# Performance work log

Hardware: AMD Instinct MI355X
Metric: run time of the kernel (lower is better)

The kernel has to match this reference:

```python
import jax, jax.numpy as jnp
import numpy as np
from functools import partial

D = 1024
H = 4 * D
E = 8
K_TOP = 2
B, T = 4, 2048
NEG_INF = jnp.float32(-1e30)


def setup_inputs() -> dict:
    key = jax.random.key(0)
    ks = jax.random.split(key, 12)
    s = 0.02
    return {
        "x": jax.random.normal(ks[0], (B, T, D), jnp.float32),
        "noise": jax.random.normal(ks[1], (B, T, E), jnp.float32),
        "gate_w": jax.random.normal(ks[2], (E, D), jnp.float32) * s,
        "gate_b": jnp.zeros((E,), jnp.float32),
        "var_w": jax.random.normal(ks[3], (E, D), jnp.float32) * s,
        "var_b": jnp.zeros((E,), jnp.float32),
        "w1": jax.random.normal(ks[4], (E, H, D), jnp.float32) * s,
        "b1": jnp.zeros((E, H), jnp.float32),
        "w2": jax.random.normal(ks[5], (E, D, H), jnp.float32) * s,
        "b2": jnp.zeros((E, D), jnp.float32),
    }


def reference(x, noise, gate_w, gate_b, var_w, var_b, w1, b1, w2, b2):
    # Noisy top-k gating
    logits = jnp.einsum("btd,ed->bte", x, gate_w) + gate_b          # [B,T,E]
    std = jax.nn.softplus(jnp.einsum("btd,ed->bte", x, var_w) + var_b)
    noisy = logits + noise * std                                      # [B,T,E]
    _, idx = jax.lax.top_k(noisy, K_TOP)                              # [B,T,K]
    # boolean top-k mask over experts
    mask = (idx[..., None] == jnp.arange(E)).any(axis=-2)             # [B,T,E]
    coef = jax.nn.softmax(jnp.where(mask, noisy, NEG_INF), axis=-1)   # zeros outside top-k

    # Combine: sum_e coef_e * FFN_e(x). coef is exactly 0 for non-selected
    # experts, so this equals the masked gather/scatter math. Scan over the
    # small expert dim to avoid a [E,B,T,H] intermediate.
    coef_e = jnp.moveaxis(coef, -1, 0)                                # [E,B,T]

    def body(acc, ew):
        w1e, b1e, w2e, b2e, ce = ew
        h = jax.nn.relu(jnp.einsum("btd,hd->bth", x, w1e) + b1e)
        y = jnp.einsum("bth,dh->btd", h, w2e) + b2e
        return acc + y * ce[..., None], None

    out, _ = jax.lax.scan(body, jnp.zeros_like(x), (w1, b1, w2, b2, coef_e))
    return out
```

## Files before the change

### kernel.cpp

```cpp
#include <hip/hip_runtime.h>
#include <hip/hip_bf16.h>
#include <math.h>

#define NTOK 8192
#define DD   1024
#define HH   4096
#define NE   8
#define SLOT_CAP 17408
#define BM 128
#define BN 128
#define BK 64

typedef __bf16 bf16;
typedef __bf16 bf16x8 __attribute__((ext_vector_type(8)));
typedef __bf16 bf16x4 __attribute__((ext_vector_type(4)));
typedef float  f32x4  __attribute__((ext_vector_type(4)));

typedef __attribute__((address_space(3))) unsigned char lds_u8;
typedef const __attribute__((address_space(1))) unsigned char g_u8;

__device__ __forceinline__ void gload16(const bf16* g, bf16* l) {
  __builtin_amdgcn_global_load_lds((g_u8*)g, (lds_u8*)l, 16, 0, 0);
}

__device__ __forceinline__ float softplus_f(float v) {
  return fmaxf(v, 0.f) + log1pf(expf(-fabsf(v)));
}

__global__ __launch_bounds__(64) void moe_gate_kernel(
    const float* __restrict__ x, const float* __restrict__ noise,
    const float* __restrict__ gate_w, const float* __restrict__ gate_b,
    const float* __restrict__ var_w,  const float* __restrict__ var_b,
    float* __restrict__ coef2, int* __restrict__ t2e, int* __restrict__ counts)
{
  const int t = blockIdx.x;
  const int lane = threadIdx.x;
  const float* xt = x + (size_t)t * DD;
  float pg[NE], pv[NE];
  #pragma unroll
  for (int e = 0; e < NE; ++e) { pg[e] = 0.f; pv[e] = 0.f; }
  #pragma unroll 4
  for (int i = 0; i < DD / 64; ++i) {
    const int d = lane + i * 64;
    const float xv = xt[d];
    #pragma unroll
    for (int e = 0; e < NE; ++e) {
      pg[e] = fmaf(xv, gate_w[e * DD + d], pg[e]);
      pv[e] = fmaf(xv, var_w[e * DD + d], pv[e]);
    }
  }
  #pragma unroll
  for (int e = 0; e < NE; ++e) {
    #pragma unroll
    for (int off = 32; off; off >>= 1) {
      pg[e] += __shfl_xor(pg[e], off);
      pv[e] += __shfl_xor(pv[e], off);
    }
  }
  if (lane == 0) {
    float noisy[NE];
    #pragma unroll
    for (int e = 0; e < NE; ++e) {
      const float lg = pg[e] + gate_b[e];
      const float sd = softplus_f(pv[e] + var_b[e]);
      noisy[e] = lg + noise[t * NE + e] * sd;
    }
    int i1 = 0; float n1 = noisy[0];
    #pragma unroll
    for (int e = 1; e < NE; ++e) if (noisy[e] > n1) { n1 = noisy[e]; i1 = e; }
    int i2 = -1; float n2 = -3.0e38f;
    #pragma unroll
    for (int e = 0; e < NE; ++e) if (e != i1 && noisy[e] > n2) { n2 = noisy[e]; i2 = e; }
    const float e2 = expf(n2 - n1);
    const float den = 1.f + e2;
    coef2[t * 2 + 0] = 1.f / den;
    coef2[t * 2 + 1] = e2 / den;
    t2e[t * 2 + 0] = i1;
    t2e[t * 2 + 1] = i2;
    atomicAdd(&counts[i1], 1);
    atomicAdd(&counts[i2], 1);
  }
}

__global__ void moe_offsets_kernel(const int* __restrict__ counts, int* __restrict__ po) {
  if (threadIdx.x == 0) {
    int acc = 0;
    po[0] = 0;
    for (int e = 0; e < NE; ++e) {
      acc += ((counts[e] + BM - 1) / BM) * BM;
      po[e + 1] = acc;
    }
  }
}

__global__ __launch_bounds__(256) void moe_scatter_kernel(
    const int* __restrict__ t2e, const float* __restrict__ coef2,
    const int* __restrict__ po, int* __restrict__ cnt2,
    int* __restrict__ assign_tok, float* __restrict__ slot_coef)
{
  const int t = blockIdx.x * 256 + threadIdx.x;
  if (t >= NTOK) return;
  #pragma unroll
  for (int k = 0; k < 2; ++k) {
    const int e = t2e[t * 2 + k];
    const int pos = atomicAdd(&cnt2[e], 1);
    const int slot = po[e] + pos;
    assign_tok[slot] = t;
    slot_coef[slot] = coef2[t * 2 + k];
  }
}

__global__ __launch_bounds__(256) void cvt_bf16_kernel(const float* __restrict__ src,
                                                       bf16* __restrict__ dst, int n4) {
  for (int i = blockIdx.x * 256 + threadIdx.x; i < n4; i += gridDim.x * 256) {
    const float4 f = ((const float4*)src)[i];
    bf16x4 v;
    v[0] = (bf16)f.x; v[1] = (bf16)f.y; v[2] = (bf16)f.z; v[3] = (bf16)f.w;
    ((bf16x4*)dst)[i] = v;
  }
}

__global__ __launch_bounds__(256) void moe_ffn1_kernel(
    const bf16* __restrict__ xb, const bf16* __restrict__ w1b, const float* __restrict__ b1,
    const int* __restrict__ assign_tok, const int* __restrict__ po,
    bf16* __restrict__ h, int chunk_base)
{
  __shared__ bf16 As[BM][BK];
  __shared__ bf16 Bs[BN][BK];
  __shared__ int toks[BM];
  const int po8 = po[NE];
  const int row0 = chunk_base + blockIdx.x * BM;
  if (row0 >= po8) return;
  int e = 0;
  while (row0 >= po[e + 1]) ++e;
  const int bn0 = blockIdx.y * BN;
  const bf16* w1e = w1b + (size_t)e * HH * DD;
  const int tid = threadIdx.x, lane = tid & 63, wave = tid >> 6;
  if (tid < BM) {
    const int s = assign_tok[row0 + tid];
    toks[tid] = s < 0 ? 0 : s;
  }
  __syncthreads();

  const int rin = lane >> 3;
  const int c8s = ((lane & 7) ^ rin) * 8;
  const bf16* asrc[4];
  const bf16* bsrc[4];
  #pragma unroll
  for (int i = 0; i < 4; ++i) {
    const int c = wave * 4 + i;
    const int row = c * 8 + rin;
    asrc[i] = xb + (size_t)toks[row] * DD + c8s;
    bsrc[i] = w1e + (size_t)(bn0 + row) * DD + c8s;
  }

  const int la = lane & 15, hi = lane >> 4;
  const int wm = (wave >> 1) * 64, wn = (wave & 1) * 64;
  f32x4 acc[4][4];
  #pragma unroll
  for (int m = 0; m < 4; ++m)
    #pragma unroll
    for (int n = 0; n < 4; ++n) acc[m][n] = {0.f, 0.f, 0.f, 0.f};

  for (int k0 = 0; k0 < DD; k0 += BK) {
    #pragma unroll
    for (int i = 0; i < 4; ++i) gload16(asrc[i] + k0, &As[(wave * 4 + i) * 8][0]);
    #pragma unroll
    for (int i = 0; i < 4; ++i) gload16(bsrc[i] + k0, &Bs[(wave * 4 + i) * 8][0]);
    __syncthreads();
    #pragma unroll
    for (int ks = 0; ks < 2; ++ks) {
      bf16x8 af[4], bff[4];
      #pragma unroll
      for (int m = 0; m < 4; ++m) {
        const int row = wm + m * 16 + la;
        const int c8 = (ks * 4 + hi) ^ (row & 7);
        af[m] = *(const bf16x8*)(&As[row][c8 * 8]);
      }
      #pragma unroll
      for (int n = 0; n < 4; ++n) {
        const int row = wn + n * 16 + la;
        const int c8 = (ks * 4 + hi) ^ (row & 7);
        bff[n] = *(const bf16x8*)(&Bs[row][c8 * 8]);
      }
      #pragma unroll
      for (int m = 0; m < 4; ++m)
        #pragma unroll
        for (int n = 0; n < 4; ++n)
          acc[m][n] = __builtin_amdgcn_mfma_f32_16x16x32_bf16(af[m], bff[n], acc[m][n], 0, 0, 0);
    }
    __syncthreads();
  }

  const int hrow0 = row0 - chunk_base;
  #pragma unroll
  for (int n = 0; n < 4; ++n) {
    const int col = bn0 + wn + n * 16 + la;
    const float bb = b1[e * HH + col];
    #pragma unroll
    for (int m = 0; m < 4; ++m) {
      const int rbase = wm + m * 16 + hi * 4;
      #pragma unroll
      for (int r = 0; r < 4; ++r) {
        float v = acc[m][n][r] + bb;
        v = v > 0.f ? v : 0.f;
        h[(size_t)(hrow0 + rbase + r) * HH + col] = (bf16)v;
      }
    }
  }
}

__global__ __launch_bounds__(256) void moe_ffn2_kernel(
    const bf16* __restrict__ h, const bf16* __restrict__ w2b, const float* __restrict__ b2,
    const int* __restrict__ assign_tok, const float* __restrict__ slot_coef,
    const int* __restrict__ po, float* __restrict__ out, int chunk_base)
{
  __shared__ bf16 As[BM][BK];
  __shared__ bf16 Bs[BN][BK];
  __shared__ int toks[BM];
  const int po8 = po[NE];
  const int row0 = chunk_base + blockIdx.x * BM;
  if (row0 >= po8) return;
  int e = 0;
  while (row0 >= po[e + 1]) ++e;
  const int bn0 = blockIdx.y * BN;
  const bf16* w2e = w2b + (size_t)e * DD * HH;
  const int tid = threadIdx.x, lane = tid & 63, wave = tid >> 6;
  if (tid < BM) toks[tid] = assign_tok[row0 + tid];
  __syncthreads();

  const int rin = lane >> 3;
  const int c8s = ((lane & 7) ^ rin) * 8;
  const bf16* asrc[4];
  const bf16* bsrc[4];
  const int arow0 = row0 - chunk_base;
  #pragma unroll
  for (int i = 0; i < 4; ++i) {
    const int c = wave * 4 + i;
    const int row = c * 8 + rin;
    asrc[i] = h + (size_t)(arow0 + row) * HH + c8s;
    bsrc[i] = w2e + (size_t)(bn0 + row) * HH + c8s;
  }

  const int la = lane & 15, hi = lane >> 4;
  const int wm = (wave >> 1) * 64, wn = (wave & 1) * 64;
  f32x4 acc[4][4];
  #pragma unroll
  for (int m = 0; m < 4; ++m)
    #pragma unroll
    for (int n = 0; n < 4; ++n) acc[m][n] = {0.f, 0.f, 0.f, 0.f};

  for (int k0 = 0; k0 < HH; k0 += BK) {
    #pragma unroll
    for (int i = 0; i < 4; ++i) gload16(asrc[i] + k0, &As[(wave * 4 + i) * 8][0]);
    #pragma unroll
    for (int i = 0; i < 4; ++i) gload16(bsrc[i] + k0, &Bs[(wave * 4 + i) * 8][0]);
    __syncthreads();
    #pragma unroll
    for (int ks = 0; ks < 2; ++ks) {
      bf16x8 af[4], bff[4];
      #pragma unroll
      for (int m = 0; m < 4; ++m) {
        const int row = wm + m * 16 + la;
        const int c8 = (ks * 4 + hi) ^ (row & 7);
        af[m] = *(const bf16x8*)(&As[row][c8 * 8]);
      }
      #pragma unroll
      for (int n = 0; n < 4; ++n) {
        const int row = wn + n * 16 + la;
        const int c8 = (ks * 4 + hi) ^ (row & 7);
        bff[n] = *(const bf16x8*)(&Bs[row][c8 * 8]);
      }
      #pragma unroll
      for (int m = 0; m < 4; ++m)
        #pragma unroll
        for (int n = 0; n < 4; ++n)
          acc[m][n] = __builtin_amdgcn_mfma_f32_16x16x32_bf16(af[m], bff[n], acc[m][n], 0, 0, 0);
    }
    __syncthreads();
  }

  #pragma unroll
  for (int n = 0; n < 4; ++n) {
    const int col = bn0 + wn + n * 16 + la;
    const float bb = b2[e * DD + col];
    #pragma unroll
    for (int m = 0; m < 4; ++m) {
      const int rbase = wm + m * 16 + hi * 4;
      #pragma unroll
      for (int r = 0; r < 4; ++r) {
        const int trow = rbase + r;
        const int tok = toks[trow];
        if (tok >= 0) {
          const float c = slot_coef[row0 + trow];
          atomicAdd(out + (size_t)tok * DD + col, c * (acc[m][n][r] + bb));
        }
      }
    }
  }
}

extern "C" void kernel_launch(void* const* d_in, const int* in_sizes, int n_in,
                              void* d_out, int out_size, void* d_ws, size_t ws_size,
                              hipStream_t stream) {
  const float* x      = (const float*)d_in[0];
  const float* noise  = (const float*)d_in[1];
  const float* gate_w = (const float*)d_in[2];
  const float* gate_b = (const float*)d_in[3];
  const float* var_w  = (const float*)d_in[4];
  const float* var_b  = (const float*)d_in[5];
  const float* w1     = (const float*)d_in[6];
  const float* b1     = (const float*)d_in[7];
  const float* w2     = (const float*)d_in[8];
  const float* b2     = (const float*)d_in[9];
  float* out = (float*)d_out;
  (void)in_sizes; (void)n_in; (void)out_size;

  char* ws = (char*)d_ws;
  size_t off = 0;
  auto alloc = [&](size_t bytes) {
    off = (off + 255) & ~(size_t)255;
    size_t o = off;
    off += bytes;
    return o;
  };
  bf16*  xb         = (bf16*)(ws + alloc((size_t)NTOK * DD * 2));
  float* coef2      = (float*)(ws + alloc((size_t)NTOK * 2 * 4));
  int*   t2e        = (int*)(ws + alloc((size_t)NTOK * 2 * 4));
  int*   counts     = (int*)(ws + alloc(64));
  int*   cnt2       = counts + 8;
  int*   po         = (int*)(ws + alloc(64));
  int*   assign_tok = (int*)(ws + alloc((size_t)SLOT_CAP * 4));
  float* slot_coef  = (float*)(ws + alloc((size_t)SLOT_CAP * 4));
  bf16*  w1b        = (bf16*)(ws + alloc((size_t)NE * HH * DD * 2));
  bf16*  w2b        = (bf16*)(ws + alloc((size_t)NE * DD * HH * 2));
  off = (off + 255) & ~(size_t)255;
  const size_t h_avail = ws_size > off ? ws_size - off : 0;
  int chunk_rows = (int)(h_avail / ((size_t)HH * 2));
  chunk_rows = (chunk_rows / BM) * BM;
  if (chunk_rows < BM) chunk_rows = BM;
  if (chunk_rows > SLOT_CAP) chunk_rows = SLOT_CAP;
  bf16* hbuf = (bf16*)(ws + off);

  hipMemsetAsync(counts, 0, 64, stream);
  hipMemsetAsync(assign_tok, 0xFF, (size_t)SLOT_CAP * 4, stream);
  hipMemsetAsync(out, 0, (size_t)NTOK * DD * 4, stream);

  moe_gate_kernel<<<NTOK, 64, 0, stream>>>(x, noise, gate_w, gate_b, var_w, var_b,
                                           coef2, t2e, counts);
  moe_offsets_kernel<<<1, 64, 0, stream>>>(counts, po);
  moe_scatter_kernel<<<NTOK / 256, 256, 0, stream>>>(t2e, coef2, po, cnt2,
                                                     assign_tok, slot_coef);
  cvt_bf16_kernel<<<2048, 256, 0, stream>>>(x, xb, NTOK * DD / 4);
  cvt_bf16_kernel<<<2048, 256, 0, stream>>>(w1, w1b, NE * HH * DD / 4);
  cvt_bf16_kernel<<<2048, 256, 0, stream>>>(w2, w2b, NE * DD * HH / 4);

  const int rounds = (SLOT_CAP + chunk_rows - 1) / chunk_rows;
  for (int r = 0; r < rounds; ++r) {
    const int cb = r * chunk_rows;
    const int rows_here = (cb + chunk_rows <= SLOT_CAP) ? chunk_rows : (SLOT_CAP - cb);
    dim3 g1(rows_here / BM, HH / BN);
    moe_ffn1_kernel<<<g1, 256, 0, stream>>>(xb, w1b, b1, assign_tok, po, hbuf, cb);
    dim3 g2(rows_here / BM, DD / BN);
    moe_ffn2_kernel<<<g2, 256, 0, stream>>>(hbuf, w2b, b2, assign_tok, slot_coef,
                                            po, out, cb);
  }
}
```

Measured before the change: 954.4 us.

## Use 256x256 double-buffered tiles with XCD-aware block remap in expert GEMMs

```diff
diff --git a/kernel.cpp b/kernel.cpp
--- a/kernel.cpp
+++ b/kernel.cpp
@@ -6,10 +6,10 @@
 #define DD   1024
 #define HH   4096
 #define NE   8
-#define SLOT_CAP 17408
-#define BM 128
-#define BN 128
+#define BM 256
+#define BN 256
 #define BK 64
+#define SLOT_CAP (2 * NTOK + NE * BM)
 
 typedef __bf16 bf16;
 typedef __bf16 bf16x8 __attribute__((ext_vector_type(8)));
@@ -120,180 +120,139 @@
   }
 }
 
-__global__ __launch_bounds__(256) void moe_ffn1_kernel(
-    const bf16* __restrict__ xb, const bf16* __restrict__ w1b, const float* __restrict__ b1,
-    const int* __restrict__ assign_tok, const int* __restrict__ po,
-    bf16* __restrict__ h, int chunk_base)
+template<int KDIM, int NCOLS, bool FFN1>
+__global__ __launch_bounds__(512, 2) void moe_gemm_kernel(
+    const bf16* __restrict__ Asrc, const bf16* __restrict__ Wsrc,
+    const float* __restrict__ bias,
+    const int* __restrict__ assign_tok, const float* __restrict__ slot_coef,
+    const int* __restrict__ po,
+    bf16* __restrict__ hout, float* __restrict__ out,
+    int chunk_base, int gx)
 {
-  __shared__ bf16 As[BM][BK];
-  __shared__ bf16 Bs[BN][BK];
+  __shared__ bf16 smA[2][BM * BK];
+  __shared__ bf16 smB[2][BN * BK];
   __shared__ int toks[BM];
+
+  const int nwg = gx * (NCOLS / BN);
+  const int lin = blockIdx.x;
+  const int q = nwg >> 3, r = nwg & 7;
+  const int xcd = lin & 7, idx = lin >> 3;
+  const int wg = (xcd < r ? xcd * (q + 1) : r * (q + 1) + (xcd - r) * q) + idx;
+  const int bx = wg % gx, by = wg / gx;
+
+  const int row0 = chunk_base + bx * BM;
   const int po8 = po[NE];
-  const int row0 = chunk_base + blockIdx.x * BM;
   if (row0 >= po8) return;
   int e = 0;
   while (row0 >= po[e + 1]) ++e;
-  const int bn0 = blockIdx.y * BN;
-  const bf16* w1e = w1b + (size_t)e * HH * DD;
-  const int tid = threadIdx.x, lane = tid & 63, wave = tid >> 6;
-  if (tid < BM) {
-    const int s = assign_tok[row0 + tid];
-    toks[tid] = s < 0 ? 0 : s;
-  }
+  const int bn0 = by * BN;
+  const bf16* We = Wsrc + (size_t)e * ((size_t)HH * DD);
+
+  const int tid = threadIdx.x, lane = tid & 63;
+  if (tid < BM) toks[tid] = assign_tok[row0 + tid];
   __syncthreads();
 
-  const int rin = lane >> 3;
-  const int c8s = ((lane & 7) ^ rin) * 8;
-  const bf16* asrc[4];
-  const bf16* bsrc[4];
+  const int t7 = tid & 7;
+  const bf16* aptr[4];
+  const bf16* bptr[4];
   #pragma unroll
   for (int i = 0; i < 4; ++i) {
-    const int c = wave * 4 + i;
-    const int row = c * 8 + rin;
-    asrc[i] = xb + (size_t)toks[row] * DD + c8s;
-    bsrc[i] = w1e + (size_t)(bn0 + row) * DD + c8s;
-  }
-
+    const int g = i * 512 + tid;
+    const int row = g >> 3;
+    const int c8 = ((t7 ^ (row & 7)) * 8);
+    int ar;
+    if constexpr (FFN1) {
+      const int s = toks[row];
+      ar = s < 0 ? 0 : s;
+    } else {
+      ar = row0 - chunk_base + row;
+    }
+    aptr[i] = Asrc + (size_t)ar * KDIM + c8;
+    bptr[i] = We + (size_t)(bn0 + row) * KDIM + c8;
+  }
+
+  auto stage = [&](int sel, int k0) {
+    #pragma unroll
+    for (int i = 0; i < 4; ++i)
+      gload16(aptr[i] + k0, &smA[sel][(i * 512 + tid) * 8]);
+    #pragma unroll
+    for (int i = 0; i < 4; ++i)
+      gload16(bptr[i] + k0, &smB[sel][(i * 512 + tid) * 8]);
+  };
+
+  const int wid = tid >> 6, wr = wid >> 2, wc = wid & 3;
   const int la = lane & 15, hi = lane >> 4;
-  const int wm = (wave >> 1) * 64, wn = (wave & 1) * 64;
-  f32x4 acc[4][4];
-  #pragma unroll
-  for (int m = 0; m < 4; ++m)
+  f32x4 acc[8][4];
+  #pragma unroll
+  for (int m = 0; m < 8; ++m)
     #pragma unroll
     for (int n = 0; n < 4; ++n) acc[m][n] = {0.f, 0.f, 0.f, 0.f};
 
-  for (int k0 = 0; k0 < DD; k0 += BK) {
-    #pragma unroll
-    for (int i = 0; i < 4; ++i) gload16(asrc[i] + k0, &As[(wave * 4 + i) * 8][0]);
-    #pragma unroll
-    for (int i = 0; i < 4; ++i) gload16(bsrc[i] + k0, &Bs[(wave * 4 + i) * 8][0]);
-    __syncthreads();
-    #pragma unroll
-    for (int ks = 0; ks < 2; ++ks) {
-      bf16x8 af[4], bff[4];
-      #pragma unroll
-      for (int m = 0; m < 4; ++m) {
-        const int row = wm + m * 16 + la;
-        const int c8 = (ks * 4 + hi) ^ (row & 7);
-        af[m] = *(const bf16x8*)(&As[row][c8 * 8]);
+  constexpr int NK = KDIM / BK;
+  stage(0, 0);
+  __syncthreads();
+  #pragma unroll 2
+  for (int ks = 0; ks < NK; ++ks) {
+    const int cur = ks & 1;
+    if (ks + 1 < NK) stage(cur ^ 1, (ks + 1) * BK);
+    const bf16* A = smA[cur];
+    const bf16* B = smB[cur];
+    #pragma unroll
+    for (int kk = 0; kk < 2; ++kk) {
+      bf16x8 af[8], bf_[4];
+      #pragma unroll
+      for (int m = 0; m < 8; ++m) {
+        const int rw = wr * 128 + m * 16 + la;
+        const int c8 = ((kk * 4 + hi) ^ (rw & 7)) * 8;
+        af[m] = *(const bf16x8*)(A + rw * 64 + c8);
       }
       #pragma unroll
       for (int n = 0; n < 4; ++n) {
-        const int row = wn + n * 16 + la;
-        const int c8 = (ks * 4 + hi) ^ (row & 7);
-        bff[n] = *(const bf16x8*)(&Bs[row][c8 * 8]);
+        const int rw = wc * 64 + n * 16 + la;
+        const int c8 = ((kk * 4 + hi) ^ (rw & 7)) * 8;
+        bf_[n] = *(const bf16x8*)(B + rw * 64 + c8);
       }
       #pragma unroll
-      for (int m = 0; m < 4; ++m)
+      for (int m = 0; m < 8; ++m)
         #pragma unroll
         for (int n = 0; n < 4; ++n)
-          acc[m][n] = __builtin_amdgcn_mfma_f32_16x16x32_bf16(af[m], bff[n], acc[m][n], 0, 0, 0);
+          acc[m][n] = __builtin_amdgcn_mfma_f32_16x16x32_bf16(af[m], bf_[n], acc[m][n], 0, 0, 0);
     }
     __syncthreads();
   }
 
-  const int hrow0 = row0 - chunk_base;
-  #pragma unroll
-  for (int n = 0; n < 4; ++n) {
-    const int col = bn0 + wn + n * 16 + la;
-    const float bb = b1[e * HH + col];
-    #pragma unroll
-    for (int m = 0; m < 4; ++m) {
-      const int rbase = wm + m * 16 + hi * 4;
-      #pragma unroll
-      for (int r = 0; r < 4; ++r) {
-        float v = acc[m][n][r] + bb;
-        v = v > 0.f ? v : 0.f;
-        h[(size_t)(hrow0 + rbase + r) * HH + col] = (bf16)v;
+  if constexpr (FFN1) {
+    #pragma unroll
+    for (int n = 0; n < 4; ++n) {
+      const int col = bn0 + wc * 64 + n * 16 + la;
+      const float bb = bias[e * NCOLS + col];
+      #pragma unroll
+      for (int m = 0; m < 8; ++m) {
+        const int rl = wr * 128 + m * 16 + hi * 4;
+        #pragma unroll
+        for (int rr = 0; rr < 4; ++rr) {
+          float v = acc[m][n][rr] + bb;
+          v = v > 0.f ? v : 0.f;
+          hout[(size_t)(row0 - chunk_base + rl + rr) * HH + col] = (bf16)v;
+        }
       }
     }
-  }
-}
-
-__global__ __launch_bounds__(256) void moe_ffn2_kernel(
-    const bf16* __restrict__ h, const bf16* __restrict__ w2b, const float* __restrict__ b2,
-    const int* __restrict__ assign_tok, const float* __restrict__ slot_coef,
-    const int* __restrict__ po, float* __restrict__ out, int chunk_base)
-{
-  __shared__ bf16 As[BM][BK];
-  __shared__ bf16 Bs[BN][BK];
-  __shared__ int toks[BM];
-  const int po8 = po[NE];
-  const int row0 = chunk_base + blockIdx.x * BM;
-  if (row0 >= po8) return;
-  int e = 0;
-  while (row0 >= po[e + 1]) ++e;
-  const int bn0 = blockIdx.y * BN;
-  const bf16* w2e = w2b + (size_t)e * DD * HH;
-  const int tid = threadIdx.x, lane = tid & 63, wave = tid >> 6;
-  if (tid < BM) toks[tid] = assign_tok[row0 + tid];
-  __syncthreads();
-
-  const int rin = lane >> 3;
-  const int c8s = ((lane & 7) ^ rin) * 8;
-  const bf16* asrc[4];
-  const bf16* bsrc[4];
-  const int arow0 = row0 - chunk_base;
-  #pragma unroll
-  for (int i = 0; i < 4; ++i) {
-    const int c = wave * 4 + i;
-    const int row = c * 8 + rin;
-    asrc[i] = h + (size_t)(arow0 + row) * HH + c8s;
-    bsrc[i] = w2e + (size_t)(bn0 + row) * HH + c8s;
-  }
-
-  const int la = lane & 15, hi = lane >> 4;
-  const int wm = (wave >> 1) * 64, wn = (wave & 1) * 64;
-  f32x4 acc[4][4];
-  #pragma unroll
-  for (int m = 0; m < 4; ++m)
-    #pragma unroll
-    for (int n = 0; n < 4; ++n) acc[m][n] = {0.f, 0.f, 0.f, 0.f};
-
-  for (int k0 = 0; k0 < HH; k0 += BK) {
-    #pragma unroll
-    for (int i = 0; i < 4; ++i) gload16(asrc[i] + k0, &As[(wave * 4 + i) * 8][0]);
-    #pragma unroll
-    for (int i = 0; i < 4; ++i) gload16(bsrc[i] + k0, &Bs[(wave * 4 + i) * 8][0]);
-    __syncthreads();
-    #pragma unroll
-    for (int ks = 0; ks < 2; ++ks) {
-      bf16x8 af[4], bff[4];
-      #pragma unroll
-      for (int m = 0; m < 4; ++m) {
-        const int row = wm + m * 16 + la;
-        const int c8 = (ks * 4 + hi) ^ (row & 7);
-        af[m] = *(const bf16x8*)(&As[row][c8 * 8]);
-      }
-      #pragma unroll
-      for (int n = 0; n < 4; ++n) {
-        const int row = wn + n * 16 + la;
-        const int c8 = (ks * 4 + hi) ^ (row & 7);
-        bff[n] = *(const bf16x8*)(&Bs[row][c8 * 8]);
-      }
-      #pragma unroll
-      for (int m = 0; m < 4; ++m)
+  } else {
+    #pragma unroll
+    for (int n = 0; n < 4; ++n) {
+      const int col = bn0 + wc * 64 + n * 16 + la;
+      const float bb = bias[e * NCOLS + col];
+      #pragma unroll
+      for (int m = 0; m < 8; ++m) {
+        const int rl = wr * 128 + m * 16 + hi * 4;
         #pragma unroll
-        for (int n = 0; n < 4; ++n)
-          acc[m][n] = __builtin_amdgcn_mfma_f32_16x16x32_bf16(af[m], bff[n], acc[m][n], 0, 0, 0);
-    }
-    __syncthreads();
-  }
-
-  #pragma unroll
-  for (int n = 0; n < 4; ++n) {
-    const int col = bn0 + wn + n * 16 + la;
-    const float bb = b2[e * DD + col];
-    #pragma unroll
-    for (int m = 0; m < 4; ++m) {
-      const int rbase = wm + m * 16 + hi * 4;
-      #pragma unroll
-      for (int r = 0; r < 4; ++r) {
-        const int trow = rbase + r;
-        const int tok = toks[trow];
-        if (tok >= 0) {
-          const float c = slot_coef[row0 + trow];
-          atomicAdd(out + (size_t)tok * DD + col, c * (acc[m][n][r] + bb));
+        for (int rr = 0; rr < 4; ++rr) {
+          const int tl = rl + rr;
+          const int tok = toks[tl];
+          if (tok >= 0) {
+            const float c = slot_coef[row0 + tl];
+            atomicAdd(out + (size_t)tok * DD + col, c * (acc[m][n][rr] + bb));
+          }
         }
       }
     }
@@ -359,10 +318,10 @@
   for (int r = 0; r < rounds; ++r) {
     const int cb = r * chunk_rows;
     const int rows_here = (cb + chunk_rows <= SLOT_CAP) ? chunk_rows : (SLOT_CAP - cb);
-    dim3 g1(rows_here / BM, HH / BN);
-    moe_ffn1_kernel<<<g1, 256, 0, stream>>>(xb, w1b, b1, assign_tok, po, hbuf, cb);
-    dim3 g2(rows_here / BM, DD / BN);
-    moe_ffn2_kernel<<<g2, 256, 0, stream>>>(hbuf, w2b, b2, assign_tok, slot_coef,
-                                            po, out, cb);
-  }
-}
+    const int gx = rows_here / BM;
+    moe_gemm_kernel<DD, HH, true><<<gx * (HH / BN), 512, 0, stream>>>(
+        xb, w1b, b1, assign_tok, slot_coef, po, hbuf, nullptr, cb, gx);
+    moe_gemm_kernel<HH, DD, false><<<gx * (DD / BN), 512, 0, stream>>>(
+        hbuf, w2b, b2, assign_tok, slot_coef, po, nullptr, out, cb, gx);
+  }
+}
```

New measurement: 995.0 us. 4.3% more time.
